# Optimization experiments

Hardware: AMD Instinct MI355X
Metric: run time of the kernel (lower is better)

Reference implementation:

```python
import jax, jax.numpy as jnp
import numpy as np
from jax import lax

B, T, L = 16, 200, 250
IDIM, ODIM, DUNITS = 512, 80, 1024
ATT_DIM, ACONV_CHANS, ACONV_K = 128, 32, 31
PRENET = 256


def setup_inputs() -> dict:
    key = jax.random.key(0)
    ks = iter(jax.random.split(key, 40))
    def nrm(shape, fan_in):
        return jax.random.normal(next(ks), shape, jnp.float32) * (fan_in ** -0.5)
    inp = {}
    inp['hs'] = jax.random.normal(next(ks), (B, T, IDIM), jnp.float32)
    inp['hlens'] = jax.random.randint(next(ks), (B,), T // 2, T + 1)
    inp['ys'] = jax.random.normal(next(ks), (B, L, ODIM), jnp.float32)
    # location-aware attention params
    inp['W_enc'] = nrm((IDIM, ATT_DIM), IDIM)
    inp['b_enc'] = jnp.zeros((ATT_DIM,), jnp.float32)
    inp['W_dec'] = nrm((DUNITS, ATT_DIM), DUNITS)
    inp['W_att'] = nrm((ACONV_CHANS, ATT_DIM), ACONV_CHANS)
    inp['loc_conv_w'] = nrm((ACONV_CHANS, 1, ACONV_K), ACONV_K)
    inp['gvec_w'] = nrm((ATT_DIM,), ATT_DIM)
    inp['gvec_b'] = jnp.zeros((), jnp.float32)
    # prenet (no bias, dropout off in eval)
    inp['prenet_W1'] = nrm((ODIM, PRENET), ODIM)
    inp['prenet_W2'] = nrm((PRENET, PRENET), PRENET)
    # LSTM cells (torch gate order i,f,g,o; bih+bhh folded into one bias)
    in0 = IDIM + PRENET
    inp['Wih0'] = nrm((4 * DUNITS, in0), in0)
    inp['Whh0'] = nrm((4 * DUNITS, DUNITS), DUNITS)
    inp['b0'] = jnp.zeros((4 * DUNITS,), jnp.float32)
    inp['Wih1'] = nrm((4 * DUNITS, DUNITS), DUNITS)
    inp['Whh1'] = nrm((4 * DUNITS, DUNITS), DUNITS)
    inp['b1'] = jnp.zeros((4 * DUNITS,), jnp.float32)
    # output heads
    inp['feat_W'] = nrm((DUNITS, ODIM), DUNITS)
    inp['prob_W'] = nrm((DUNITS,), DUNITS)
    inp['prob_b'] = jnp.zeros((), jnp.float32)
    # postnet: conv(no bias) + BN(eval; running mean=0, var=1 folded away) + tanh
    inp['post_w_in'] = nrm((512, ODIM, 5), 5 * ODIM)
    inp['post_g_in'] = jnp.ones((512,), jnp.float32)
    inp['post_b_in'] = jnp.zeros((512,), jnp.float32)
    inp['post_w_mid'] = nrm((3, 512, 512, 5), 5 * 512)
    inp['post_g_mid'] = jnp.ones((3, 512), jnp.float32)
    inp['post_b_mid'] = jnp.zeros((3, 512), jnp.float32)
    inp['post_w_out'] = nrm((ODIM, 512, 5), 5 * 512)
    inp['post_g_out'] = jnp.ones((ODIM,), jnp.float32)
    inp['post_b_out'] = jnp.zeros((ODIM,), jnp.float32)
    return inp


def _conv1d(x, w, pad):
    # x: [B, Cin, T], w: [Cout, Cin, K]
    return lax.conv_general_dilated(x, w, (1,), [(pad, pad)],
                                    dimension_numbers=('NCH', 'OIH', 'NCH'))


def _lstm(x, h, c, Wih, Whh, b):
    g = x @ Wih.T + h @ Whh.T + b
    i, f, gg, o = jnp.split(g, 4, axis=-1)
    c2 = jax.nn.sigmoid(f) * c + jax.nn.sigmoid(i) * jnp.tanh(gg)
    return jax.nn.sigmoid(o) * jnp.tanh(c2), c2


def reference(hs, hlens, ys, W_enc, b_enc, W_dec, W_att, loc_conv_w, gvec_w, gvec_b,
              prenet_W1, prenet_W2, Wih0, Whh0, b0, Wih1, Whh1, b1,
              feat_W, prob_W, prob_b,
              post_w_in, post_g_in, post_b_in, post_w_mid, post_g_mid, post_b_mid,
              post_w_out, post_g_out, post_b_out):
    mask = jnp.arange(T)[None, :] < hlens[:, None]            # [B,T]
    pre_enc = hs @ W_enc + b_enc                              # [B,T,A] precomputed
    # teacher forcing: prenet input at step i is ys[:, i-1] (zeros at i=0);
    # prenet has no recurrent dependency -> vectorize over time
    prev = jnp.concatenate([jnp.zeros((B, 1, ODIM), hs.dtype), ys[:, :L - 1]], axis=1)
    pren = jax.nn.relu(jax.nn.relu(prev @ prenet_W1) @ prenet_W2)  # [B,L,256]
    att_w0 = mask.astype(hs.dtype) / hlens[:, None].astype(hs.dtype)
    z = jnp.zeros((B, DUNITS), hs.dtype)
    carry0 = (z, z, z, z, att_w0)

    def step(carry, pren_t):
        z0, c0, z1, c1, att_w = carry
        conv = _conv1d(att_w[:, None, :], loc_conv_w, ACONV_K // 2)   # [B,C,T]
        e = jnp.tanh(pre_enc + jnp.einsum('bct,ca->bta', conv, W_att)
                     + (z0 @ W_dec)[:, None, :]) @ gvec_w + gvec_b    # [B,T]
        e = jnp.where(mask, e, -1e30)
        w = jax.nn.softmax(2.0 * e, axis=1)                           # scaling=2.0
        att_c = jnp.einsum('bt,btd->bd', w, hs)
        x = jnp.concatenate([att_c, pren_t], axis=1)
        z0n, c0n = _lstm(x, z0, c0, Wih0, Whh0, b0)
        z1n, c1n = _lstm(z0n, z1, c1, Wih1, Whh1, b1)
        return (z0n, c0n, z1n, c1n, w), (z1n @ feat_W, z1n @ prob_W + prob_b)

    _, (outs, probs) = lax.scan(step, carry0, jnp.swapaxes(pren, 0, 1))
    outs = jnp.transpose(outs, (1, 2, 0))   # [B, odim, L] (matches torch.stack dim=2)
    probs = probs.T                         # [B, L]
    # postnet (BN in eval with running mean=0/var=1 reduces to gamma*x+beta)
    h = jnp.tanh(post_g_in[:, None] * _conv1d(outs, post_w_in, 2) + post_b_in[:, None])
    for i in range(3):
        h = jnp.tanh(post_g_mid[i][:, None] * _conv1d(h, post_w_mid[i], 2)
                     + post_b_mid[i][:, None])
    h = post_g_out[:, None] * _conv1d(h, post_w_out, 2) + post_b_out[:, None]
    post_outs = outs + h
    return jnp.swapaxes(post_outs, 1, 2), jnp.swapaxes(outs, 1, 2), probs
```

## Files before the change

### kernel.cpp

```cpp
#include <hip/hip_runtime.h>
#include <cstdint>
#include <cstddef>

constexpr int B_ = 16, T_ = 200, L_ = 250;
constexpr int IDIM = 512, ODIM = 80, DUNITS = 1024;
constexpr int ADIM = 128, ACH = 32, AK = 31;
constexpr int PRE = 256;
constexpr int TPAD = 208;

typedef _Float16 h16;
typedef _Float16 half8 __attribute__((ext_vector_type(8)));
typedef _Float16 half4 __attribute__((ext_vector_type(4)));
typedef float f32x4 __attribute__((ext_vector_type(4)));

constexpr int FSTEP = 800;
constexpr int FZ0W = 0, FDPW = 256, FAW = 288;

constexpr size_t OFF_PE    = 0;
constexpr size_t OFF_H0H   = 851968;
constexpr size_t OFF_Z1H   = 917504;
constexpr size_t OFF_ATTC  = 983040;
constexpr size_t OFF_DP    = 999424;
constexpr size_t OFF_FLAGS = 1007616;
constexpr size_t OFF_XT1   = 1807616;
constexpr size_t OFF_XTA   = 2888960;
constexpr size_t OFF_XTB   = 7214336;
constexpr size_t ZERO_BYTES= 11539712;
constexpr size_t OFF_MB    = 11539712;
constexpr size_t OFF_WDR   = 11547904;
constexpr size_t OFF_PREN  = 11810048;
constexpr size_t OFF_HSH   = 13858048;
constexpr size_t OFF_W0AH  = 17134848;
constexpr size_t OFF_WHH0  = 23426304;
constexpr size_t OFF_WI1   = 31814912;
constexpr size_t OFF_WHH1  = 40203520;
constexpr size_t OFF_Z1ALL = 48592128;
constexpr size_t OFF_WTIN  = 56784128;
constexpr size_t OFF_WTMID = 57439488;
constexpr size_t OFF_WTOUT = 65303808;
constexpr size_t OFF_YSP   = 65713408;
constexpr size_t OFF_H1P   = 66481408;
constexpr size_t OFF_W1P   = 68529408;
constexpr size_t OFF_W2P   = 68578560;
constexpr size_t OFF_WENCP = 68709632;
constexpr size_t OFF_FWP   = 68840704;

__device__ __forceinline__ float fsig(float x) {
  x = fminf(fmaxf(x, -30.f), 30.f);
  return __builtin_amdgcn_rcpf(1.f + __expf(-x));
}
__device__ __forceinline__ float ftanh(float x) {
  x = fminf(fmaxf(x, -15.f), 15.f);
  const float e = __expf(2.f * x);
  return (e - 1.f) * __builtin_amdgcn_rcpf(e + 1.f);
}
__device__ __forceinline__ f32x4 mfma16(half8 a, half8 b, f32x4 c) {
  return __builtin_amdgcn_mfma_f32_16x16x32_f16(a, b, c, 0, 0, 0);
}
__device__ __forceinline__ half8 load8_agent(const h16* p) {
  union { unsigned long long q[2]; half8 v; } cv;
  cv.q[0] = __hip_atomic_load((const unsigned long long*)p, __ATOMIC_RELAXED,
                              __HIP_MEMORY_SCOPE_AGENT);
  cv.q[1] = __hip_atomic_load(((const unsigned long long*)p) + 1, __ATOMIC_RELAXED,
                              __HIP_MEMORY_SCOPE_AGENT);
  return cv.v;
}
__device__ __forceinline__ float loadf_agent(const float* p) {
  union { unsigned u; float f; } cv;
  cv.u = __hip_atomic_load((const unsigned*)p, __ATOMIC_RELAXED,
                           __HIP_MEMORY_SCOPE_AGENT);
  return cv.f;
}
__device__ __forceinline__ void storef_agent(float* p, float v) {
  union { unsigned u; float f; } cv; cv.f = v;
  __hip_atomic_store((unsigned*)p, cv.u, __ATOMIC_RELAXED, __HIP_MEMORY_SCOPE_AGENT);
}
__device__ __forceinline__ int loadw(const int* p) {
  return __hip_atomic_load(p, __ATOMIC_RELAXED, __HIP_MEMORY_SCOPE_AGENT);
}
__device__ __forceinline__ void storew(int* p, int v) {
  __hip_atomic_store(p, v, __ATOMIC_RELAXED, __HIP_MEMORY_SCOPE_AGENT);
}
__device__ __forceinline__ void poll_n(const int* base, const int n) {
  if ((int)threadIdx.x < n) {
    const int* f = base + threadIdx.x;
    while (loadw(f) == 0) __builtin_amdgcn_s_sleep(1);
  }
  __syncthreads();
  __builtin_amdgcn_sched_barrier(0);
}
__device__ __forceinline__ void poll_all256(const int* base) {
  const int* f = base + threadIdx.x;
  while (loadw(f) == 0) __builtin_amdgcn_s_sleep(1);
  __syncthreads();
  __builtin_amdgcn_sched_barrier(0);
}


__global__ void k_zero(float4* __restrict__ p, int n4) {
  const int i = blockIdx.x * blockDim.x + threadIdx.x;
  if (i < n4) p[i] = make_float4(0.f, 0.f, 0.f, 0.f);
}

__global__ void k_precMb(const float* __restrict__ lconv, const float* __restrict__ W_att,
                         h16* __restrict__ Mb) {
  const int at = blockIdx.x, lane = threadIdx.x;
  const int a = at * 16 + (lane & 15);
  const int k0 = (lane >> 4) * 8;
  half8 o;
#pragma unroll
  for (int j = 0; j < 8; ++j) {
    const int k = k0 + j;
    float v = 0.f;
    if (k < AK)
      for (int c = 0; c < ACH; ++c) v += lconv[c * AK + k] * W_att[c * ADIM + a];
    o[j] = (h16)v;
  }
  *(half8*)(Mb + (size_t)(at * 64 + lane) * 8) = o;
}

__global__ void k_cvt_perm(const float* __restrict__ src, h16* __restrict__ dst,
                           const int K) {
  const int rr = blockIdx.x;
  const int u = rr >> 2, g = rr & 3;
  const float* s = src + (size_t)(g * 1024 + u) * K;
  h16* d = dst + (size_t)rr * K;
  for (int k = threadIdx.x; k < K; k += 256) d[k] = (h16)s[k];
}

__global__ void k_cvt_wdec(const float* __restrict__ Wdec, h16* __restrict__ Wdr) {
  const int a = blockIdx.x;
  for (int k = threadIdx.x; k < 1024; k += 256)
    Wdr[(size_t)a * 1024 + k] = (h16)Wdec[(size_t)k * ADIM + a];
}

__global__ void k_cvt_f32f16(const float* __restrict__ src, h16* __restrict__ dst) {
  const size_t i = ((size_t)blockIdx.x * 256 + threadIdx.x) * 4;
  const float4 v = *(const float4*)(src + i);
  half4 o; o[0] = (h16)v.x; o[1] = (h16)v.y; o[2] = (h16)v.z; o[3] = (h16)v.w;
  *(half4*)(dst + i) = o;
}

__global__ void k_cvt_wpin(const float* __restrict__ w, h16* __restrict__ o) {
  const int co = blockIdx.x;
  for (int i = threadIdx.x; i < 640; i += 256) {
    const int k = i >> 7, ci = i & 127;
    o[(size_t)co * 640 + i] = (ci < 80) ? (h16)w[((size_t)co * 80 + ci) * 5 + k] : (h16)0.f;
  }
}
__global__ void k_cvt_wpmid(const float* __restrict__ w, h16* __restrict__ o) {
  const int idx = blockIdx.x;
  const float* s = w + (size_t)idx * 512 * 5;
  h16* d = o + (size_t)idx * 2560;
  for (int i = threadIdx.x; i < 2560; i += 256) {
    const int k = i >> 9, ci = i & 511;
    d[i] = (h16)s[(size_t)ci * 5 + k];
  }
}
__global__ void k_cvt_wpout(const float* __restrict__ w, h16* __restrict__ o) {
  const int co = blockIdx.x;
  for (int i = threadIdx.x; i < 2560; i += 256) {
    const int k = i >> 9, ci = i & 511;
    o[(size_t)co * 2560 + i] = (h16)w[((size_t)co * 512 + ci) * 5 + k];
  }
}

__global__ void k_p_ys(const float* __restrict__ ys, h16* __restrict__ ysp) {
  const int m = blockIdx.x;
  const int l = m >> 4, b = m & 15;
  const int co = threadIdx.x;
  h16 v = (h16)0.f;
  if (l > 0 && co < 80) v = (h16)ys[((size_t)b * L_ + (l - 1)) * ODIM + co];
  ysp[(size_t)m * 96 + co] = v;
}
__global__ void k_p_w1(const float* __restrict__ W1, h16* __restrict__ W1p) {
  const int p = blockIdx.x;
  const int o = threadIdx.x;
  W1p[(size_t)p * 96 + o] = (o < 80) ? (h16)W1[(size_t)o * PRE + p] : (h16)0.f;
}
__global__ void k_p_w2(const float* __restrict__ W2, h16* __restrict__ W2p) {
  const int p2 = blockIdx.x;
  const int p = threadIdx.x;
  W2p[(size_t)p2 * 256 + p] = (h16)W2[(size_t)p * PRE + p2];
}
__global__ void k_p_wenc(const float* __restrict__ We, h16* __restrict__ Wp) {
  const int a = blockIdx.x;
  for (int d = threadIdx.x; d < 512; d += 256)
    Wp[(size_t)a * 512 + d] = (h16)We[(size_t)d * ADIM + a];
}
__global__ void k_p_fw(const float* __restrict__ fw, const float* __restrict__ pw,
                       h16* __restrict__ Wp) {
  const int co = blockIdx.x;
  for (int d = threadIdx.x; d < 1024; d += 256) {
    h16 v = (h16)0.f;
    if (co < 80) v = (h16)fw[(size_t)d * ODIM + co];
    else if (co == 80) v = (h16)pw[d];
    Wp[(size_t)co * 1024 + d] = v;
  }
}

template <int KCH, int EPI>
__global__ void __launch_bounds__(256) k_gemw(const h16* __restrict__ A,
    const h16* __restrict__ W, h16* __restrict__ dsth, float* __restrict__ dstf,
    float* __restrict__ dstf2, const float* __restrict__ bvec) {
  constexpr int KA = KCH * 32;
  const int m0 = blockIdx.x * 16, n0 = blockIdx.y * 64;
  const int lane = threadIdx.x & 63, wave = threadIdx.x >> 6;
  const int nloc = lane & 15, kl8 = (lane >> 4) * 8;
  const h16* wr = W + (size_t)(n0 + wave * 16 + nloc) * KA + kl8;
  half8 w[KCH];
#pragma unroll
  for (int c = 0; c < KCH; ++c) w[c] = *(const half8*)(wr + c * 32);
  const h16* ar = A + (size_t)(m0 + nloc) * KA + kl8;
  f32x4 acc = {0.f, 0.f, 0.f, 0.f};
#pragma unroll
  for (int c = 0; c < KCH; ++c)
    acc = mfma16(*(const half8*)(ar + c * 32), w[c], acc);
  const int n = n0 + wave * 16 + (lane & 15);
#pragma unroll
  for (int r = 0; r < 4; ++r) {
    const int m = m0 + 4 * (lane >> 4) + r;
    const float v = acc[r];
    if (EPI == 0) {
      dsth[(size_t)m * 256 + n] = (h16)fmaxf(v, 0.f);
    } else if (EPI == 1) {
      const int b = m / 200, t = m % 200;
      dsth[((size_t)b * 128 + n) * TPAD + t] = (h16)(v + bvec[n]);
    } else {
      const int b = m & 15, l = m >> 4;
      if (n < 80) {
        dstf[((size_t)b * L_ + l) * ODIM + n] = v;
        dsth[((size_t)b * 264 + l + 2) * 128 + n] = (h16)v;
      } else if (n == 80) {
        dstf2[(size_t)b * L_ + l] = v + bvec[0];
      }
    }
  }
}

template <int CIP, int NK, bool TANH, bool FINAL>
__global__ void __launch_bounds__(256) k_cvmf(const h16* __restrict__ xT,
    const h16* __restrict__ wT, const float* __restrict__ gamma,
    const float* __restrict__ beta, h16* __restrict__ yT,
    const float* __restrict__ res, float* __restrict__ out0) {
  __shared__ float s_red[4][64][5];
  __shared__ float s_g[16][20];
  constexpr int KTOT = NK * 128;
  const int l0 = blockIdx.x * 16, co0 = blockIdx.y * 16;
  const int tid = threadIdx.x, lane = tid & 63, wave = tid >> 6;
  const int nloc = lane & 15, kl8 = (lane >> 4) * 8;
  const h16* wr = wT + (size_t)(co0 + nloc) * KTOT + wave * (NK * 32) + kl8;
  half8 w[NK];
#pragma unroll
  for (int c = 0; c < NK; ++c) w[c] = *(const half8*)(wr + c * 32);
  for (int b = 0; b < B_; ++b) {
    f32x4 acc = {0.f, 0.f, 0.f, 0.f};
    const h16* xb = xT + (size_t)b * 264 * CIP;
#pragma unroll
    for (int c = 0; c < NK; ++c) {
      const int kg = wave * (NK * 32) + c * 32;
      const int k = kg / CIP, ci = kg & (CIP - 1);
      const half8 a = *(const half8*)(xb + (size_t)(l0 + nloc + k) * CIP + ci + kl8);
      acc = mfma16(a, w[c], acc);
    }
#pragma unroll
    for (int r = 0; r < 4; ++r) s_red[wave][lane][r] = acc[r];
    __syncthreads();
    {
      const float v = s_red[0][lane][wave] + s_red[1][lane][wave]
                    + s_red[2][lane][wave] + s_red[3][lane][wave];
      s_g[lane & 15][4 * (lane >> 4) + wave] = v;
    }
    __syncthreads();
    {
      const int co_l = tid & 15, l_l = tid >> 4;
      const int co = co0 + co_l, l = l0 + l_l;
      if (l < L_ && tid < 256) {
        float v = gamma[co] * s_g[co_l][l_l] + beta[co];
        if (TANH) v = ftanh(v);
        if (FINAL) {
          const size_t o = ((size_t)b * L_ + l) * ODIM + co;
          out0[o] = res[o] + v;
        } else {
          yT[((size_t)b * 264 + l + 2) * 512 + co] = (h16)v;
        }
      }
    }
    __syncthreads();
  }
}


struct ScanP {
  const h16 *pe_h, *Mb, *Wdr, *hs_h, *pren_h;
  const h16 *W0ah, *Whh0h, *Wz01h, *Whh1h;
  h16 *h0h, *z1h, *attc;
  float *dp;
  const float *gvw, *b0, *b1;
  const int *hlens;
  h16 *z1all;
  int *flags;
};

__device__ __forceinline__ void lstm0_partA(const h16* pren_t, const h16* z0p,
    const half8 wA[6], const half8 wH[8], f32x4& acc) {
  const int lane = threadIdx.x & 63, wave = threadIdx.x >> 6;
  const int nloc = lane & 15, kl8 = (lane >> 4) * 8;
  half8 rz[8];
#pragma unroll
  for (int c = 0; c < 8; ++c)
    rz[c] = load8_agent(z0p + nloc * DUNITS + wave * 256 + c * 32 + kl8);
#pragma unroll
  for (int c = 0; c < 8; ++c) acc = mfma16(rz[c], wH[c], acc);
#pragma unroll
  for (int c = 0; c < 6; ++c) {
    const int kg = wave * 192 + c * 32;
    if (kg >= 512)
      acc = mfma16(*(const half8*)(pren_t + nloc * PRE + (kg - 512) + kl8), wA[c], acc);
  }
}

__device__ __forceinline__ void lstm0_partB(const ScanP& P,
    h16* z0o, const int slab, const half8 wA[6], float& c0reg, f32x4 acc,
    float sred[4][64][5], float sg[16][20], h16* sho) {
  const int tid = threadIdx.x;
  const int lane = tid & 63, wave = tid >> 6;
  const int nloc = lane & 15, kl8 = (lane >> 4) * 8;
  half8 ra[6];
#pragma unroll
  for (int c = 0; c < 6; ++c) {
    const int kg = wave * 192 + c * 32;
    if (kg < 512) ra[c] = load8_agent(P.attc + nloc * IDIM + kg + kl8);
  }
#pragma unroll
  for (int c = 0; c < 6; ++c) {
    const int kg = wave * 192 + c * 32;
    if (kg < 512) acc = mfma16(ra[c], wA[c], acc);
  }
#pragma unroll
  for (int r = 0; r < 4; ++r) sred[wave][lane][r] = acc[r];
  __syncthreads();
  {
    const float v = sred[0][lane][wave] + sred[1][lane][wave]
                  + sred[2][lane][wave] + sred[3][lane][wave];
    sg[lane & 15][4 * (lane >> 4) + wave] = v;
  }
  __syncthreads();
  if (tid < 64) {
    const int ul = tid >> 4, b = tid & 15;
    const int u = slab * 4 + ul;
    const float xi = sg[ul * 4 + 0][b] + P.b0[u];
    const float xf = sg[ul * 4 + 1][b] + P.b0[1024 + u];
    const float xg = sg[ul * 4 + 2][b] + P.b0[2048 + u];
    const float xo = sg[ul * 4 + 3][b] + P.b0[3072 + u];
    const float cn = fsig(xf) * c0reg + fsig(xi) * ftanh(xg);
    c0reg = cn;
    sho[ul * 16 + b] = (h16)(fsig(xo) * ftanh(cn));
  }
  __syncthreads();
  if (tid < 16) {
    union { h16 h[4]; unsigned long long q; } u4;
#pragma unroll
    for (int j = 0; j < 4; ++j) u4.h[j] = sho[j * 16 + tid];
    __hip_atomic_store((unsigned long long*)(z0o + tid * DUNITS + slab * 4), u4.q,
                       __ATOMIC_RELAXED, __HIP_MEMORY_SCOPE_AGENT);
  }
}

__device__ __forceinline__ void lstm1_mm(const ScanP& P, const half8 r0[8],
    const half8 r1[8], h16* z1o, h16* z1all_s, const int slab,
    const half8 wI[8], const half8 wHH[8], float& c1reg,
    float sred[4][64][5], float sg[16][20], h16* sho) {
  const int tid = threadIdx.x;
  const int lane = tid & 63, wave = tid >> 6;
  f32x4 acc = {0.f, 0.f, 0.f, 0.f};
#pragma unroll
  for (int c = 0; c < 8; ++c) acc = mfma16(r0[c], wI[c], acc);
#pragma unroll
  for (int c = 0; c < 8; ++c) acc = mfma16(r1[c], wHH[c], acc);
#pragma unroll
  for (int r = 0; r < 4; ++r) sred[wave][lane][r] = acc[r];
  __syncthreads();
  {
    const float v = sred[0][lane][wave] + sred[1][lane][wave]
                  + sred[2][lane][wave] + sred[3][lane][wave];
    sg[lane & 15][4 * (lane >> 4) + wave] = v;
  }
  __syncthreads();
  if (tid < 64) {
    const int ul = tid >> 4, b = tid & 15;
    const int u = slab * 4 + ul;
    const float xi = sg[ul * 4 + 0][b] + P.b1[u];
    const float xf = sg[ul * 4 + 1][b] + P.b1[1024 + u];
    const float xg = sg[ul * 4 + 2][b] + P.b1[2048 + u];
    const float xo = sg[ul * 4 + 3][b] + P.b1[3072 + u];
    const float cn = fsig(xf) * c1reg + fsig(xi) * ftanh(xg);
    c1reg = cn;
    const float hn = fsig(xo) * ftanh(cn);
    const h16 hh = (h16)hn;
    z1all_s[b * DUNITS + u] = hh;
    sho[ul * 16 + b] = hh;
  }
  __syncthreads();
  if (tid < 16) {
    union { h16 h[4]; unsigned long long q; } u4;
#pragma unroll
    for (int j = 0; j < 4; ++j) u4.h[j] = sho[j * 16 + tid];
    __hip_atomic_store((unsigned long long*)(z1o + tid * DUNITS + slab * 4), u4.q,
                       __ATOMIC_RELAXED, __HIP_MEMORY_SCOPE_AGENT);
  }
}

__global__ void __launch_bounds__(256, 1) k_scan(const ScanP P) {
  __shared__ float s_red[4][64][5];
  __shared__ float s_g[16][20];
  __shared__ h16   s_ho[64];
  __shared__ float s_aw[240];
  __shared__ float s_dp[ADIM];
  __shared__ float s_gv[ADIM];
  __shared__ float s_ew[256];
  __shared__ float s_wt[208];
  __shared__ float s_par[4][512];
  __shared__ float s_r8[8];
  __shared__ float s_bc[2];
  __shared__ float s_cvpe[13][8][64][4];

  const int blk = blockIdx.x, tid = threadIdx.x;
  const int lane = tid & 63, wave = tid >> 6;
  constexpr int BD = B_ * DUNITS;

  if (blk < 16) {
    const int b = blk;
    const int hl = P.hlens[b];
    const int mtmax = (hl + 15) >> 4;
    const int slab = 240 + b;
    const int l15 = lane & 15;
    half8 bfrag[8];
#pragma unroll
    for (int at = 0; at < 8; ++at)
      bfrag[at] = *(const half8*)(P.Mb + (size_t)(at * 64 + lane) * 8);
    half8 wA[6], wH[8];
    {
      const int nloc = lane & 15, kl8 = (lane >> 4) * 8;
      const h16* wrA = P.W0ah + ((size_t)(slab * 16 + nloc)) * 768 + wave * 192 + kl8;
      const h16* wrH = P.Whh0h + ((size_t)(slab * 16 + nloc)) * 1024 + wave * 256 + kl8;
#pragma unroll
      for (int c = 0; c < 6; ++c) wA[c] = *(const half8*)(wrA + c * 32);
#pragma unroll
      for (int c = 0; c < 8; ++c) wH[c] = *(const half8*)(wrH + c * 32);
    }
    if (tid < 240) {
      const int tt = tid - 15;
      s_aw[tid] = (tt >= 0 && tt < hl) ? (1.f / (float)hl) : 0.f;
    }
    if (tid < ADIM) s_gv[tid] = P.gvw[tid];
    __syncthreads();
    float c0reg = 0.f;

    for (int mi = 0; mi < 4; ++mi) {
      const int mt = wave + mi * 4;
      if (mt < mtmax) {
        half8 af;
#pragma unroll
        for (int j = 0; j < 8; ++j)
          af[j] = (h16)s_aw[mt * 16 + l15 + (lane >> 4) * 8 + j];
        const int t0 = mt * 16 + 4 * (lane >> 4);
        half4 pe[8];
#pragma unroll
        for (int at = 0; at < 8; ++at)
          pe[at] = *(const half4*)(P.pe_h + ((size_t)b * ADIM + at * 16 + l15) * TPAD + t0);
#pragma unroll
        for (int at = 0; at < 8; ++at) {
          f32x4 z4 = {0.f, 0.f, 0.f, 0.f};
          const f32x4 cv = mfma16(af, bfrag[at], z4);
          float4 o;
          o.x = cv[0] + (float)pe[at][0]; o.y = cv[1] + (float)pe[at][1];
          o.z = cv[2] + (float)pe[at][2]; o.w = cv[3] + (float)pe[at][3];
          *(float4*)&s_cvpe[mt][at][lane][0] = o;
        }
      }
    }
    __syncthreads();

    for (int i = 0; i < L_; ++i) {
      const h16* z0p = P.h0h + (size_t)(i & 1) * BD;
      h16* z0o = P.h0h + (size_t)((i & 1) ^ 1) * BD;
      int* sf = P.flags + (size_t)i * FSTEP;
      poll_n(sf + FDPW, 8);
      if (tid < ADIM) s_dp[tid] = loadf_agent(P.dp + b * ADIM + tid);
      __syncthreads();
#pragma unroll
      for (int mi = 0; mi < 4; ++mi) {
        const int mt = wave + mi * 4;
        if (mt < mtmax) {
          const int t0 = mt * 16 + 4 * (lane >> 4);
          float e0 = 0.f, e1 = 0.f, e2 = 0.f, e3 = 0.f;
#pragma unroll
          for (int at = 0; at < 8; ++at) {
            const float4 v = *(const float4*)&s_cvpe[mt][at][lane][0];
            const int a = at * 16 + l15;
            const float g = s_gv[a], d = s_dp[a];
            e0 += g * ftanh(v.x + d);
            e1 += g * ftanh(v.y + d);
            e2 += g * ftanh(v.z + d);
            e3 += g * ftanh(v.w + d);
          }
#pragma unroll
          for (int o = 1; o < 16; o <<= 1) {
            e0 += __shfl_xor(e0, o); e1 += __shfl_xor(e1, o);
            e2 += __shfl_xor(e2, o); e3 += __shfl_xor(e3, o);
          }
          if (l15 == 0) {
            s_ew[t0 + 0] = e0; s_ew[t0 + 1] = e1; s_ew[t0 + 2] = e2; s_ew[t0 + 3] = e3;
          }
        }
      }
      __syncthreads();
      const float val = (tid < hl) ? 2.f * s_ew[tid] : -3.0e38f;
      float m = val;
#pragma unroll
      for (int o = 32; o > 0; o >>= 1) m = fmaxf(m, __shfl_xor(m, o));
      if ((tid & 63) == 0) s_r8[tid >> 6] = m;
      __syncthreads();
      if (tid == 0) s_bc[0] = fmaxf(fmaxf(s_r8[0], s_r8[1]), fmaxf(s_r8[2], s_r8[3]));
      __syncthreads();
      const float pp = (tid < hl) ? __expf(val - s_bc[0]) : 0.f;
      float ssum = pp;
#pragma unroll
      for (int o = 32; o > 0; o >>= 1) ssum += __shfl_xor(ssum, o);
      if ((tid & 63) == 0) s_r8[4 + (tid >> 6)] = ssum;
      __syncthreads();
      if (tid == 0) s_bc[1] = __builtin_amdgcn_rcpf(s_r8[4] + s_r8[5] + s_r8[6] + s_r8[7]);
      __syncthreads();
      if (tid < T_) {
        const float w = pp * s_bc[1];
        s_wt[tid] = w;
        s_aw[15 + tid] = w;
      }
      __syncthreads();
      const h16* hsb = P.hs_h + (size_t)b * T_ * IDIM;
      {
        const int d0 = lane * 8;
        const h16* hp = hsb + d0;
        float a8[8] = {0.f, 0.f, 0.f, 0.f, 0.f, 0.f, 0.f, 0.f};
        int tt = wave;
        for (; tt + 12 < hl; tt += 16) {
          const half8 h0 = *(const half8*)(hp + (size_t)tt * IDIM);
          const half8 h1 = *(const half8*)(hp + (size_t)(tt + 4) * IDIM);
          const half8 h2 = *(const half8*)(hp + (size_t)(tt + 8) * IDIM);
          const half8 h3 = *(const half8*)(hp + (size_t)(tt + 12) * IDIM);
          const float w0 = s_wt[tt], w1 = s_wt[tt + 4];
          const float w2 = s_wt[tt + 8], w3 = s_wt[tt + 12];
#pragma unroll
          for (int j = 0; j < 8; ++j)
            a8[j] += w0 * (float)h0[j] + w1 * (float)h1[j]
                   + w2 * (float)h2[j] + w3 * (float)h3[j];
        }
        for (; tt < hl; tt += 4) {
          const half8 hv = *(const half8*)(hp + (size_t)tt * IDIM);
          const float wt = s_wt[tt];
#pragma unroll
          for (int j = 0; j < 8; ++j) a8[j] += wt * (float)hv[j];
        }
#pragma unroll
        for (int j = 0; j < 8; ++j) s_par[wave][d0 + j] = a8[j];
      }
      __syncthreads();
      {
        const int d = tid * 2;
        const float cx0 = s_par[0][d] + s_par[1][d] + s_par[2][d] + s_par[3][d];
        const float cx1 = s_par[0][d + 1] + s_par[1][d + 1] + s_par[2][d + 1]
                        + s_par[3][d + 1];
        union { h16 h[2]; unsigned u; } cv;
        cv.h[0] = (h16)cx0; cv.h[1] = (h16)cx1;
        __hip_atomic_store((unsigned*)(P.attc + b * IDIM + d), cv.u,
                           __ATOMIC_RELAXED, __HIP_MEMORY_SCOPE_AGENT);
      }
      asm volatile("s_waitcnt vmcnt(0)" ::: "memory");
      __syncthreads();
      if (tid < 16) storew(sf + FAW + tid * 32 + b, 1);
      f32x4 acc0 = {0.f, 0.f, 0.f, 0.f};
      lstm0_partA(P.pren_h + (size_t)i * (B_ * PRE), z0p, wA, wH, acc0);
      poll_n(sf + FAW + (blk & 15) * 32, 16);
      lstm0_partB(P, z0o, slab, wA, c0reg, acc0, s_red, s_g, s_ho);
      asm volatile("s_waitcnt vmcnt(0)" ::: "memory");
      __syncthreads();
      if (tid == 0) storew(sf + FZ0W + blk, 1);
      for (int mi = 0; mi < 4; ++mi) {
        const int mt = wave + mi * 4;
        if (mt < mtmax) {
          half8 af;
#pragma unroll
          for (int j = 0; j < 8; ++j)
            af[j] = (h16)s_aw[mt * 16 + l15 + (lane >> 4) * 8 + j];
          const int t0 = mt * 16 + 4 * (lane >> 4);
          half4 pe[8];
#pragma unroll
          for (int at = 0; at < 8; ++at)
            pe[at] = *(const half4*)(P.pe_h + ((size_t)b * ADIM + at * 16 + l15) * TPAD + t0);
#pragma unroll
          for (int at = 0; at < 8; ++at) {
            f32x4 z4 = {0.f, 0.f, 0.f, 0.f};
            const f32x4 cv = mfma16(af, bfrag[at], z4);
            float4 o;
            o.x = cv[0] + (float)pe[at][0]; o.y = cv[1] + (float)pe[at][1];
            o.z = cv[2] + (float)pe[at][2]; o.w = cv[3] + (float)pe[at][3];
            *(float4*)&s_cvpe[mt][at][lane][0] = o;
          }
        }
      }
      __syncthreads();
    }
    return;
  }

  const int g = blk - 16;
  const bool dbl = (g < 16);
  const bool isdp = (g >= 16 && g < 24);
  half8 wA0[6], wH0[8], wI1a[8], wHH1a[8], wI1b[8], wHH1b[8], wD[8];
  {
    const int nloc = lane & 15, kl8 = (lane >> 4) * 8;
    const h16* wrA = P.W0ah + ((size_t)(g * 16 + nloc)) * 768 + wave * 192 + kl8;
    const h16* wrH = P.Whh0h + ((size_t)(g * 16 + nloc)) * 1024 + wave * 256 + kl8;
    const h16* wrI = P.Wz01h + ((size_t)(g * 16 + nloc)) * 1024 + wave * 256 + kl8;
    const h16* wrX = P.Whh1h + ((size_t)(g * 16 + nloc)) * 1024 + wave * 256 + kl8;
#pragma unroll
    for (int c = 0; c < 6; ++c) wA0[c] = *(const half8*)(wrA + c * 32);
#pragma unroll
    for (int c = 0; c < 8; ++c) wH0[c] = *(const half8*)(wrH + c * 32);
#pragma unroll
    for (int c = 0; c < 8; ++c) wI1a[c] = *(const half8*)(wrI + c * 32);
#pragma unroll
    for (int c = 0; c < 8; ++c) wHH1a[c] = *(const half8*)(wrX + c * 32);
    if (dbl) {
      const h16* wrI2 = P.Wz01h + ((size_t)((240 + g) * 16 + nloc)) * 1024 + wave * 256 + kl8;
      const h16* wrX2 = P.Whh1h + ((size_t)((240 + g) * 16 + nloc)) * 1024 + wave * 256 + kl8;
#pragma unroll
      for (int c = 0; c < 8; ++c) wI1b[c] = *(const half8*)(wrI2 + c * 32);
#pragma unroll
      for (int c = 0; c < 8; ++c) wHH1b[c] = *(const half8*)(wrX2 + c * 32);
    }
    if (isdp) {
      const h16* wrD = P.Wdr + ((size_t)((g - 16) * 16 + nloc)) * 1024 + wave * 256 + kl8;
#pragma unroll
      for (int c = 0; c < 8; ++c) wD[c] = *(const half8*)(wrD + c * 32);
    }
  }
  float c0reg = 0.f, c1a = 0.f, c1b = 0.f;
  const int nloc = lane & 15, kl8 = (lane >> 4) * 8;

  for (int i = 0; i < L_; ++i) {
    const h16* z0p = P.h0h + (size_t)(i & 1) * BD;
    h16* z0o = P.h0h + (size_t)((i & 1) ^ 1) * BD;
    const h16* z1p = P.z1h + (size_t)((i & 1) ^ 1) * BD;
    h16* z1o = P.z1h + (size_t)(i & 1) * BD;
    int* sf = P.flags + (size_t)i * FSTEP;
    if (i > 0) poll_all256(P.flags + (size_t)(i - 1) * FSTEP + FZ0W);
    if (isdp) {
      half8 rz[8];
#pragma unroll
      for (int c = 0; c < 8; ++c)
        rz[c] = load8_agent(z0p + nloc * DUNITS + wave * 256 + c * 32 + kl8);
      f32x4 acc = {0.f, 0.f, 0.f, 0.f};
#pragma unroll
      for (int c = 0; c < 8; ++c) acc = mfma16(rz[c], wD[c], acc);
#pragma unroll
      for (int r = 0; r < 4; ++r) s_red[wave][lane][r] = acc[r];
      __syncthreads();
      {
        const float v = s_red[0][lane][wave] + s_red[1][lane][wave]
                      + s_red[2][lane][wave] + s_red[3][lane][wave];
        const int row = lane & 15, batch = 4 * (lane >> 4) + wave;
        storef_agent(P.dp + batch * ADIM + (g - 16) * 16 + row, v);
      }
      asm volatile("s_waitcnt vmcnt(0)" ::: "memory");
      __syncthreads();
      if (tid == 0) storew(sf + FDPW + (g - 16), 1);
    }
    if (i > 0) {
      half8 r0[8], r1[8];
#pragma unroll
      for (int c = 0; c < 8; ++c)
        r0[c] = load8_agent(z0p + nloc * DUNITS + wave * 256 + c * 32 + kl8);
#pragma unroll
      for (int c = 0; c < 8; ++c)
        r1[c] = load8_agent(z1p + nloc * DUNITS + wave * 256 + c * 32 + kl8);
      h16* z1s = P.z1all + (size_t)(i - 1) * BD;
      lstm1_mm(P, r0, r1, z1o, z1s, g, wI1a, wHH1a, c1a, s_red, s_g, s_ho);
      if (dbl)
        lstm1_mm(P, r0, r1, z1o, z1s, 240 + g, wI1b, wHH1b, c1b, s_red, s_g, s_ho);
    }
    f32x4 acc0 = {0.f, 0.f, 0.f, 0.f};
    lstm0_partA(P.pren_h + (size_t)i * (B_ * PRE), z0p, wA0, wH0, acc0);
    poll_n(sf + FAW + (blk & 15) * 32, 16);
    lstm0_partB(P, z0o, g, wA0, c0reg, acc0, s_red, s_g, s_ho);
    asm volatile("s_waitcnt vmcnt(0)" ::: "memory");
    __syncthreads();
    if (tid == 0) storew(sf + FZ0W + blk, 1);
  }
  poll_all256(P.flags + (size_t)(L_ - 1) * FSTEP + FZ0W);
  {
    const h16* z0p = P.h0h + (size_t)(L_ & 1) * BD;
    const h16* z1p = P.z1h + (size_t)((L_ & 1) ^ 1) * BD;
    h16* z1o = P.z1h + (size_t)(L_ & 1) * BD;
    h16* z1s = P.z1all + (size_t)(L_ - 1) * BD;
    half8 r0[8], r1[8];
#pragma unroll
    for (int c = 0; c < 8; ++c)
      r0[c] = load8_agent(z0p + nloc * DUNITS + wave * 256 + c * 32 + kl8);
#pragma unroll
    for (int c = 0; c < 8; ++c)
      r1[c] = load8_agent(z1p + nloc * DUNITS + wave * 256 + c * 32 + kl8);
    lstm1_mm(P, r0, r1, z1o, z1s, g, wI1a, wHH1a, c1a, s_red, s_g, s_ho);
    if (dbl)
      lstm1_mm(P, r0, r1, z1o, z1s, 240 + g, wI1b, wHH1b, c1b, s_red, s_g, s_ho);
  }
}


extern "C" void kernel_launch(void* const* d_in, const int* in_sizes, int n_in,
                              void* d_out, int out_size, void* d_ws, size_t ws_size,
                              hipStream_t stream) {
  const float* hs    = (const float*)d_in[0];
  const int*   hlens = (const int*)d_in[1];
  const float* ys    = (const float*)d_in[2];
  const float* W_enc = (const float*)d_in[3];
  const float* b_enc = (const float*)d_in[4];
  const float* W_dec = (const float*)d_in[5];
  const float* W_att = (const float*)d_in[6];
  const float* lconv = (const float*)d_in[7];
  const float* gvw   = (const float*)d_in[8];
  const float* pW1   = (const float*)d_in[10];
  const float* pW2   = (const float*)d_in[11];
  const float* Wih0  = (const float*)d_in[12];
  const float* Whh0  = (const float*)d_in[13];
  const float* b0    = (const float*)d_in[14];
  const float* Wih1  = (const float*)d_in[15];
  const float* Whh1  = (const float*)d_in[16];
  const float* b1    = (const float*)d_in[17];
  const float* featW = (const float*)d_in[18];
  const float* probW = (const float*)d_in[19];
  const float* probB = (const float*)d_in[20];
  const float* pwin  = (const float*)d_in[21];
  const float* pgin  = (const float*)d_in[22];
  const float* pbin  = (const float*)d_in[23];
  const float* pwmid = (const float*)d_in[24];
  const float* pgmid = (const float*)d_in[25];
  const float* pbmid = (const float*)d_in[26];
  const float* pwout = (const float*)d_in[27];
  const float* pgout = (const float*)d_in[28];
  const float* pbout = (const float*)d_in[29];

  char* ws = (char*)d_ws;
  h16*   pe_h   = (h16*)(ws + OFF_PE);
  h16*   h0h    = (h16*)(ws + OFF_H0H);
  h16*   z1h    = (h16*)(ws + OFF_Z1H);
  h16*   attc_h = (h16*)(ws + OFF_ATTC);
  float* dp     = (float*)(ws + OFF_DP);
  int*   flags  = (int*)(ws + OFF_FLAGS);
  h16*   xT1    = (h16*)(ws + OFF_XT1);
  h16*   xTA    = (h16*)(ws + OFF_XTA);
  h16*   xTB    = (h16*)(ws + OFF_XTB);
  h16*   Mb     = (h16*)(ws + OFF_MB);
  h16*   Wdr    = (h16*)(ws + OFF_WDR);
  h16*   pren_h = (h16*)(ws + OFF_PREN);
  h16*   hs_h   = (h16*)(ws + OFF_HSH);
  h16*   W0ah   = (h16*)(ws + OFF_W0AH);
  h16*   Whh0h  = (h16*)(ws + OFF_WHH0);
  h16*   Wz01h  = (h16*)(ws + OFF_WI1);
  h16*   Whh1h  = (h16*)(ws + OFF_WHH1);
  h16*   z1all  = (h16*)(ws + OFF_Z1ALL);
  h16*   wTin   = (h16*)(ws + OFF_WTIN);
  h16*   wTmid  = (h16*)(ws + OFF_WTMID);
  h16*   wTout  = (h16*)(ws + OFF_WTOUT);
  h16*   ysp    = (h16*)(ws + OFF_YSP);
  h16*   h1p    = (h16*)(ws + OFF_H1P);
  h16*   W1p    = (h16*)(ws + OFF_W1P);
  h16*   W2p    = (h16*)(ws + OFF_W2P);
  h16*   Wencp  = (h16*)(ws + OFF_WENCP);
  h16*   featWp = (h16*)(ws + OFF_FWP);

  float* out0 = (float*)d_out;
  float* out1 = out0 + (size_t)B_ * L_ * ODIM;
  float* out2 = out1 + (size_t)B_ * L_ * ODIM;

  hipLaunchKernelGGL(k_zero, dim3((ZERO_BYTES / 16 + 255) / 256), dim3(256), 0, stream,
                     (float4*)ws, (int)(ZERO_BYTES / 16));
  hipLaunchKernelGGL(k_precMb, dim3(8), dim3(64), 0, stream, lconv, W_att, Mb);
  hipLaunchKernelGGL(k_cvt_perm, dim3(4096), dim3(256), 0, stream, Wih0, W0ah, 768);
  hipLaunchKernelGGL(k_cvt_perm, dim3(4096), dim3(256), 0, stream, Whh0, Whh0h, 1024);
  hipLaunchKernelGGL(k_cvt_perm, dim3(4096), dim3(256), 0, stream, Wih1, Wz01h, 1024);
  hipLaunchKernelGGL(k_cvt_perm, dim3(4096), dim3(256), 0, stream, Whh1, Whh1h, 1024);
  hipLaunchKernelGGL(k_cvt_wdec, dim3(128), dim3(256), 0, stream, W_dec, Wdr);
  hipLaunchKernelGGL(k_cvt_f32f16, dim3(1600), dim3(256), 0, stream, hs, hs_h);
  hipLaunchKernelGGL(k_cvt_wpin, dim3(512), dim3(256), 0, stream, pwin, wTin);
  hipLaunchKernelGGL(k_cvt_wpmid, dim3(3 * 512), dim3(256), 0, stream, pwmid, wTmid);
  hipLaunchKernelGGL(k_cvt_wpout, dim3(80), dim3(256), 0, stream, pwout, wTout);
  hipLaunchKernelGGL(k_p_ys, dim3(4000), dim3(96), 0, stream, ys, ysp);
  hipLaunchKernelGGL(k_p_w1, dim3(256), dim3(96), 0, stream, pW1, W1p);
  hipLaunchKernelGGL(k_p_w2, dim3(256), dim3(256), 0, stream, pW2, W2p);
  hipLaunchKernelGGL(k_p_wenc, dim3(128), dim3(256), 0, stream, W_enc, Wencp);
  hipLaunchKernelGGL(k_p_fw, dim3(128), dim3(256), 0, stream, featW, probW, featWp);

  hipLaunchKernelGGL((k_gemw<16, 1>), dim3(200, 2), dim3(256), 0, stream,
                     hs_h, Wencp, pe_h, nullptr, nullptr, b_enc);
  hipLaunchKernelGGL((k_gemw<3, 0>), dim3(250, 4), dim3(256), 0, stream,
                     ysp, W1p, h1p, nullptr, nullptr, nullptr);
  hipLaunchKernelGGL((k_gemw<8, 0>), dim3(250, 4), dim3(256), 0, stream,
                     h1p, W2p, pren_h, nullptr, nullptr, nullptr);

  ScanP S{pe_h, Mb, Wdr, hs_h, pren_h, W0ah, Whh0h, Wz01h, Whh1h,
          h0h, z1h, attc_h, dp, gvw, b0, b1, hlens, z1all, flags};
  hipLaunchKernelGGL(k_scan, dim3(256), dim3(256), 0, stream, S);

  hipLaunchKernelGGL((k_gemw<32, 2>), dim3(250, 2), dim3(256), 0, stream,
                     z1all, featWp, xT1, out1, out2, probB);

  hipLaunchKernelGGL((k_cvmf<128, 5, true, false>), dim3(16, 32), dim3(256), 0, stream,
                     xT1, wTin, pgin, pbin, xTA, nullptr, nullptr);
  hipLaunchKernelGGL((k_cvmf<512, 20, true, false>), dim3(16, 32), dim3(256), 0, stream,
                     xTA, wTmid, pgmid, pbmid, xTB, nullptr, nullptr);
  hipLaunchKernelGGL((k_cvmf<512, 20, true, false>), dim3(16, 32), dim3(256), 0, stream,
                     xTB, wTmid + (size_t)512 * 2560, pgmid + 512, pbmid + 512,
                     xTA, nullptr, nullptr);
  hipLaunchKernelGGL((k_cvmf<512, 20, true, false>), dim3(16, 32), dim3(256), 0, stream,
                     xTA, wTmid + (size_t)2 * 512 * 2560, pgmid + 1024, pbmid + 1024,
                     xTB, nullptr, nullptr);
  hipLaunchKernelGGL((k_cvmf<512, 20, false, true>), dim3(16, 5), dim3(256), 0, stream,
                     xTB, wTout, pgout, pbout, nullptr, out1, out0);
}
```

Before: 5.802 ms.

## Compute decoder attention projection locally in attention blocks instead of separate dp blocks

Each attention block now holds the full W_dec projection for its 128 attention dims in registers (64 half8 fragments per lane). Every step it computes z0·W_dec itself with MFMAs, reading all 16 batch rows of z0. Previously 8 dedicated blocks computed dp, wrote it to global memory and raised flags. This removes one cross-block flag handoff and a global round trip per step. In exchange, each attention block does 16x redundant work and reads all of z0, and the large register footprint may cause spills or lower occupancy.

```diff
diff --git a/kernel.cpp b/kernel.cpp
--- a/kernel.cpp
+++ b/kernel.cpp
@@ -14,7 +14,7 @@
 typedef float f32x4 __attribute__((ext_vector_type(4)));
 
 constexpr int FSTEP = 800;
-constexpr int FZ0W = 0, FDPW = 256, FAW = 288;
+constexpr int FZ0W = 0, FAW = 288;
 
 constexpr size_t OFF_PE    = 0;
 constexpr size_t OFF_H0H   = 851968;
@@ -65,16 +65,6 @@
                               __HIP_MEMORY_SCOPE_AGENT);
   return cv.v;
 }
-__device__ __forceinline__ float loadf_agent(const float* p) {
-  union { unsigned u; float f; } cv;
-  cv.u = __hip_atomic_load((const unsigned*)p, __ATOMIC_RELAXED,
-                           __HIP_MEMORY_SCOPE_AGENT);
-  return cv.f;
-}
-__device__ __forceinline__ void storef_agent(float* p, float v) {
-  union { unsigned u; float f; } cv; cv.f = v;
-  __hip_atomic_store((unsigned*)p, cv.u, __ATOMIC_RELAXED, __HIP_MEMORY_SCOPE_AGENT);
-}
 __device__ __forceinline__ int loadw(const int* p) {
   return __hip_atomic_load(p, __ATOMIC_RELAXED, __HIP_MEMORY_SCOPE_AGENT);
 }
@@ -295,7 +285,6 @@
   const h16 *pe_h, *Mb, *Wdr, *hs_h, *pren_h;
   const h16 *W0ah, *Whh0h, *Wz01h, *Whh1h;
   h16 *h0h, *z1h, *attc;
-  float *dp;
   const float *gvw, *b0, *b1;
   const int *hlens;
   h16 *z1all;
@@ -435,19 +424,28 @@
     const int mtmax = (hl + 15) >> 4;
     const int slab = 240 + b;
     const int l15 = lane & 15;
+    const int nloc = lane & 15, kl8 = (lane >> 4) * 8;
     half8 bfrag[8];
 #pragma unroll
     for (int at = 0; at < 8; ++at)
       bfrag[at] = *(const half8*)(P.Mb + (size_t)(at * 64 + lane) * 8);
     half8 wA[6], wH[8];
     {
-      const int nloc = lane & 15, kl8 = (lane >> 4) * 8;
       const h16* wrA = P.W0ah + ((size_t)(slab * 16 + nloc)) * 768 + wave * 192 + kl8;
       const h16* wrH = P.Whh0h + ((size_t)(slab * 16 + nloc)) * 1024 + wave * 256 + kl8;
 #pragma unroll
       for (int c = 0; c < 6; ++c) wA[c] = *(const half8*)(wrA + c * 32);
 #pragma unroll
       for (int c = 0; c < 8; ++c) wH[c] = *(const half8*)(wrH + c * 32);
+    }
+    half8 wd0[32], wd1[32];
+    {
+      const h16* wr0 = P.Wdr + (size_t)(wave * 32 + nloc) * 1024 + kl8;
+      const h16* wr1 = P.Wdr + (size_t)(wave * 32 + 16 + nloc) * 1024 + kl8;
+#pragma unroll
+      for (int c = 0; c < 32; ++c) wd0[c] = *(const half8*)(wr0 + c * 32);
+#pragma unroll
+      for (int c = 0; c < 32; ++c) wd1[c] = *(const half8*)(wr1 + c * 32);
     }
     if (tid < 240) {
       const int tt = tid - 15;
@@ -486,8 +484,26 @@
       const h16* z0p = P.h0h + (size_t)(i & 1) * BD;
       h16* z0o = P.h0h + (size_t)((i & 1) ^ 1) * BD;
       int* sf = P.flags + (size_t)i * FSTEP;
-      poll_n(sf + FDPW, 8);
-      if (tid < ADIM) s_dp[tid] = loadf_agent(P.dp + b * ADIM + tid);
+      if (i > 0) poll_all256(P.flags + (size_t)(i - 1) * FSTEP + FZ0W);
+      {
+        f32x4 da0 = {0.f, 0.f, 0.f, 0.f}, da1 = {0.f, 0.f, 0.f, 0.f};
+#pragma unroll
+        for (int c0 = 0; c0 < 32; c0 += 8) {
+          half8 rz[8];
+#pragma unroll
+          for (int j = 0; j < 8; ++j)
+            rz[j] = load8_agent(z0p + nloc * DUNITS + (c0 + j) * 32 + kl8);
+#pragma unroll
+          for (int j = 0; j < 8; ++j) {
+            da0 = mfma16(rz[j], wd0[c0 + j], da0);
+            da1 = mfma16(rz[j], wd1[c0 + j], da1);
+          }
+        }
+        if ((lane >> 4) == (b >> 2)) {
+          s_dp[wave * 32 + l15]      = da0[b & 3];
+          s_dp[wave * 32 + 16 + l15] = da1[b & 3];
+        }
+      }
       __syncthreads();
 #pragma unroll
       for (int mi = 0; mi < 4; ++mi) {
@@ -616,8 +632,7 @@
 
   const int g = blk - 16;
   const bool dbl = (g < 16);
-  const bool isdp = (g >= 16 && g < 24);
-  half8 wA0[6], wH0[8], wI1a[8], wHH1a[8], wI1b[8], wHH1b[8], wD[8];
+  half8 wA0[6], wH0[8], wI1a[8], wHH1a[8], wI1b[8], wHH1b[8];
   {
     const int nloc = lane & 15, kl8 = (lane >> 4) * 8;
     const h16* wrA = P.W0ah + ((size_t)(g * 16 + nloc)) * 768 + wave * 192 + kl8;
@@ -639,11 +654,6 @@
       for (int c = 0; c < 8; ++c) wI1b[c] = *(const half8*)(wrI2 + c * 32);
 #pragma unroll
       for (int c = 0; c < 8; ++c) wHH1b[c] = *(const half8*)(wrX2 + c * 32);
-    }
-    if (isdp) {
-      const h16* wrD = P.Wdr + ((size_t)((g - 16) * 16 + nloc)) * 1024 + wave * 256 + kl8;
-#pragma unroll
-      for (int c = 0; c < 8; ++c) wD[c] = *(const half8*)(wrD + c * 32);
     }
   }
   float c0reg = 0.f, c1a = 0.f, c1b = 0.f;
@@ -656,27 +666,6 @@
     h16* z1o = P.z1h + (size_t)(i & 1) * BD;
     int* sf = P.flags + (size_t)i * FSTEP;
     if (i > 0) poll_all256(P.flags + (size_t)(i - 1) * FSTEP + FZ0W);
-    if (isdp) {
-      half8 rz[8];
-#pragma unroll
-      for (int c = 0; c < 8; ++c)
-        rz[c] = load8_agent(z0p + nloc * DUNITS + wave * 256 + c * 32 + kl8);
-      f32x4 acc = {0.f, 0.f, 0.f, 0.f};
-#pragma unroll
-      for (int c = 0; c < 8; ++c) acc = mfma16(rz[c], wD[c], acc);
-#pragma unroll
-      for (int r = 0; r < 4; ++r) s_red[wave][lane][r] = acc[r];
-      __syncthreads();
-      {
-        const float v = s_red[0][lane][wave] + s_red[1][lane][wave]
-                      + s_red[2][lane][wave] + s_red[3][lane][wave];
-        const int row = lane & 15, batch = 4 * (lane >> 4) + wave;
-        storef_agent(P.dp + batch * ADIM + (g - 16) * 16 + row, v);
-      }
-      asm volatile("s_waitcnt vmcnt(0)" ::: "memory");
-      __syncthreads();
-      if (tid == 0) storew(sf + FDPW + (g - 16), 1);
-    }
     if (i > 0) {
       half8 r0[8], r1[8];
 #pragma unroll
@@ -756,7 +745,6 @@
   h16*   h0h    = (h16*)(ws + OFF_H0H);
   h16*   z1h    = (h16*)(ws + OFF_Z1H);
   h16*   attc_h = (h16*)(ws + OFF_ATTC);
-  float* dp     = (float*)(ws + OFF_DP);
   int*   flags  = (int*)(ws + OFF_FLAGS);
   h16*   xT1    = (h16*)(ws + OFF_XT1);
   h16*   xTA    = (h16*)(ws + OFF_XTA);
@@ -810,7 +798,7 @@
                      h1p, W2p, pren_h, nullptr, nullptr, nullptr);
 
   ScanP S{pe_h, Mb, Wdr, hs_h, pren_h, W0ah, Whh0h, Wz01h, Whh1h,
-          h0h, z1h, attc_h, dp, gvw, b0, b1, hlens, z1all, flags};
+          h0h, z1h, attc_h, gvw, b0, b1, hlens, z1all, flags};
   hipLaunchKernelGGL(k_scan, dim3(256), dim3(256), 0, stream, S);
 
   hipLaunchKernelGGL((k_gemw<32, 2>), dim3(250, 2), dim3(256), 0, stream,
```

Result: slower. 7.465 ms (+28.7%).
